# Kernel tuning notes

Hardware: AMD Instinct MI355X
Metric: run time of the kernel (lower is better)

The kernel has to match this reference:

```python
import jax, jax.numpy as jnp
import numpy as np

NUM_EMBEDDINGS = 1024
EMBEDDING_DIM = 256
COMMITMENT_COST = 0.25


def setup_inputs() -> dict:
    key = jax.random.key(0)
    k1, k2 = jax.random.split(key)
    x = jax.random.normal(k1, (16, 4096, EMBEDDING_DIM), dtype=jnp.float32)
    # torch init: uniform(-1/K, 1/K); keep same scale
    embedding_weight = jax.random.uniform(
        k2, (NUM_EMBEDDINGS, EMBEDDING_DIM), dtype=jnp.float32,
        minval=-1.0 / NUM_EMBEDDINGS, maxval=1.0 / NUM_EMBEDDINGS)
    return {"x": x, "embedding_weight": embedding_weight}


def reference(x, embedding_weight):
    original_shape = x.shape
    x_flat = x.reshape(-1, EMBEDDING_DIM)                     # [N, D]
    d2 = (jnp.sum(x_flat ** 2, axis=1, keepdims=True)
          + jnp.sum(embedding_weight ** 2, axis=1)
          - 2.0 * x_flat @ embedding_weight.T)                # [N, K]
    d2 = jnp.maximum(d2, 0.0)
    encoding_indices = jnp.argmin(d2, axis=1)                 # [N]
    quantized_flat = embedding_weight[encoding_indices]        # [N, D]
    quantized = quantized_flat.reshape(original_shape)

    q_sg = jax.lax.stop_gradient(quantized)
    codebook_loss = jnp.mean((q_sg - x) ** 2)
    commitment_loss = jnp.mean((x - q_sg) ** 2)
    vq_total_loss = codebook_loss + COMMITMENT_COST * commitment_loss

    # straight-through estimator
    quantized_st = x + jax.lax.stop_gradient(quantized - x)

    # perplexity via index counts (avoids materializing one-hot [N, K])
    n = x_flat.shape[0]
    counts = jnp.zeros((NUM_EMBEDDINGS,), jnp.float32).at[encoding_indices].add(1.0)
    avg_probs = counts / n
    perplexity = jnp.exp(-jnp.sum(avg_probs * jnp.log(avg_probs + 1e-10)))

    return quantized_st, vq_total_loss, perplexity, encoding_indices
```

## Files before the change

kernel.cpp:

```cpp
#include <hip/hip_runtime.h>
#include <math.h>

#define N_ROWS   65536
#define DIM      256
#define KCODES   1024
#define Q_SIZE   (N_ROWS * DIM)
#define OUT_LOSS Q_SIZE
#define OUT_PERP (Q_SIZE + 1)
#define OUT_IDX  (Q_SIZE + 2)

#define TAUP 200.0f

#define WS_LOSS   0
#define WS_RCNT   8
#define WS_E2     16
#define WS_E2P    4112
#define WS_COUNTS 8208
#define WS_IDX    12304
#define WS_RLIST  274448
#define WS_ET     536592
#define WS_P      1585168

typedef _Float16 half8 __attribute__((ext_vector_type(8)));
typedef _Float16 half4 __attribute__((ext_vector_type(4)));
typedef float    f32x4 __attribute__((ext_vector_type(4)));

#define ROWB 528
#define RPB  64

#define LDS_X  0
#define LDS_E2 33792

__global__ void k_prep(const float* __restrict__ E, float* __restrict__ e2,
                       float* __restrict__ e2p, float* __restrict__ Et,
                       _Float16* __restrict__ P,
                       int* __restrict__ counts, double* __restrict__ loss,
                       int* __restrict__ rcnt) {
    int b = blockIdx.x, t = threadIdx.x;
    __shared__ double red[256];
    float v = E[b * DIM + t];
    red[t] = (double)v * (double)v;

    {
        int o   = b * 256 + t;
        int j    = o & 7;
        int lane = (o >> 3) & 63;
        int nt   = (o >> 9) & 3;
        int kk   = (o >> 11) & 7;
        int cbq  = o >> 14;
        int q = cbq >> 2, cb = cbq & 3;
        int code = q * 256 + cb * 64 + nt * 16 + (lane & 15);
        int d    = (lane >> 4) * 8 + kk * 32 + j;
        P[o] = (_Float16)(E[code * DIM + d] * 1024.0f);
    }

    __syncthreads();
    for (int s = 128; s > 0; s >>= 1) {
        if (t < s) red[t] += red[t + s];
        __syncthreads();
    }
    if (t == 0) { e2[b] = (float)red[0]; e2p[b] = (float)(red[0] * 1048576.0); }

    int o = b * 256 + t;
    int d = o >> 10, k = o & 1023;
    Et[o] = E[k * DIM + d];

    if (b < 4) counts[b * 256 + t] = 0;
    if (b == 0 && t == 0) { *loss = 0.0; *rcnt = 0; }
}

__global__ void __launch_bounds__(256)
k_main(const float* __restrict__ X, const _Float16* __restrict__ P,
       const float* __restrict__ e2p,
       int* __restrict__ idx_ws, int* __restrict__ rlist,
       int* __restrict__ rcnt) {
    __shared__ __align__(16) char sAll[37888];
    const int tid  = threadIdx.x;
    const int wid  = tid >> 6;
    const int lane = tid & 63;
    const int c16  = lane & 15;
    const int kg   = lane >> 4;
    const int rb   = blockIdx.x * RPB;

    char* sA = sAll + LDS_X;

    {
        const f32x4* Xg = (const f32x4*)(X + (size_t)rb * DIM);
        #pragma unroll
        for (int it = 0; it < 16; ++it) {
            int f = it * 256 + tid;
            int row = f >> 6, d4 = f & 63;
            f32x4 v = __builtin_nontemporal_load(&Xg[(size_t)row * 64 + d4]);
            half4 hh = {(_Float16)v[0], (_Float16)v[1], (_Float16)v[2], (_Float16)v[3]};
            *(half4*)(sA + row * ROWB + d4 * 8) = hh;
        }
        ((f32x4*)(sAll + LDS_E2))[tid] = ((const f32x4*)e2p)[tid];
    }
    __syncthreads();

    const char* gB = (const char*)P + (size_t)wid * 131072 + (size_t)lane * 16;
#define GLOADC(dst, c)                                                        \
    asm volatile("global_load_dwordx4 %0, %1, off"                            \
                 : "=v"(dst)                                                  \
                 : "v"(gB + (size_t)((c) * 1024)))
#define VMW(n) { asm volatile("s_waitcnt vmcnt(" #n ")" ::: "memory");        \
                 __builtin_amdgcn_sched_barrier(0); }

    int Abase[4];
    #pragma unroll
    for (int mt = 0; mt < 4; ++mt) Abase[mt] = (mt * 16 + c16) * ROWB + kg * 16;

    float tb1[16], tb2[16];
    int   ti1[16];
    #pragma unroll
    for (int i = 0; i < 16; ++i) { tb1[i] = 3.4e38f; tb2[i] = 3.4e38f; ti1[i] = 0; }

    const int cw = wid * 256;
    const float* sE2 = (const float*)(sAll + LDS_E2);

    f32x4 acc[4][4];

    half8 b[3][4];
    #pragma unroll
    for (int nt = 0; nt < 4; ++nt) GLOADC(b[0][nt], 0 * 4 + nt);
    #pragma unroll
    for (int nt = 0; nt < 4; ++nt) GLOADC(b[1][nt], 1 * 4 + nt);
    __builtin_amdgcn_sched_barrier(0);

    #pragma unroll
    for (int s = 0; s < 32; ++s) {
        const int kk = s & 7;
        if (kk == 0) {
            #pragma unroll
            for (int mt = 0; mt < 4; ++mt)
                #pragma unroll
                for (int nt = 0; nt < 4; ++nt) acc[mt][nt] = 0.0f;
        }
        if (s <= 29) {
            #pragma unroll
            for (int nt = 0; nt < 4; ++nt) GLOADC(b[(s + 2) % 3][nt], (s + 2) * 4 + nt);
        }
        if (s <= 29)      VMW(8)
        else if (s == 30) VMW(4)
        else              VMW(0)

        half8 ah[4];
        #pragma unroll
        for (int mt = 0; mt < 4; ++mt)
            ah[mt] = *(const half8*)(sA + Abase[mt] + kk * 64);

        #pragma unroll
        for (int mt = 0; mt < 4; ++mt) {
            acc[mt][0] = __builtin_amdgcn_mfma_f32_16x16x32_f16(ah[mt], b[s % 3][0], acc[mt][0], 0, 0, 0);
            acc[mt][1] = __builtin_amdgcn_mfma_f32_16x16x32_f16(ah[mt], b[s % 3][1], acc[mt][1], 0, 0, 0);
            acc[mt][2] = __builtin_amdgcn_mfma_f32_16x16x32_f16(ah[mt], b[s % 3][2], acc[mt][2], 0, 0, 0);
            acc[mt][3] = __builtin_amdgcn_mfma_f32_16x16x32_f16(ah[mt], b[s % 3][3], acc[mt][3], 0, 0, 0);
        }

        if (kk == 7) {
            const int cb = s >> 3;
            const int cbase = cw + cb * 64;
            const int c0 = cbase + c16;
            float e2v[4];
            #pragma unroll
            for (int nt = 0; nt < 4; ++nt) e2v[nt] = sE2[c0 + nt * 16];
            #pragma unroll
            for (int mt = 0; mt < 4; ++mt)
                #pragma unroll
                for (int nt = 0; nt < 4; ++nt) {
                    int code = cbase + nt * 16 + c16;
                    #pragma unroll
                    for (int r = 0; r < 4; ++r) {
                        float sc = fmaf(-2048.0f, acc[mt][nt][r], e2v[nt]);
                        int ix = mt * 4 + r;
                        tb2[ix] = __builtin_amdgcn_fmed3f(tb1[ix], tb2[ix], sc);
                        bool lt = sc < tb1[ix];
                        tb1[ix] = lt ? sc : tb1[ix];
                        ti1[ix] = lt ? code : ti1[ix];
                    }
                }
        }
    }
#undef GLOADC
#undef VMW

    #pragma unroll
    for (int ix = 0; ix < 16; ++ix) {
        float v1 = tb1[ix], v2 = tb2[ix];
        int   j1 = ti1[ix];
        #pragma unroll
        for (int m = 1; m < 16; m <<= 1) {
            float ov1 = __shfl_xor(v1, m, 64);
            int   oj1 = __shfl_xor(j1, m, 64);
            float ov2 = __shfl_xor(v2, m, 64);
            bool take = (ov1 < v1) || (ov1 == v1 && oj1 < j1);
            float losr = take ? v1 : ov1;
            v1 = take ? ov1 : v1;
            j1 = take ? oj1 : j1;
            v2 = fminf(fminf(v2, ov2), losr);
        }
        tb1[ix] = v1; tb2[ix] = v2; ti1[ix] = j1;
    }

    __syncthreads();
    float* mB1 = (float*)sA;
    float* mB2 = (float*)(sA + 1024);
    int*   mI1 = (int*)(sA + 2048);
    #pragma unroll
    for (int ix = 0; ix < 16; ++ix) {
        if (c16 == ix) {
            int row = (ix >> 2) * 16 + kg * 4 + (ix & 3);
            mB1[row * 4 + wid] = tb1[ix];
            mB2[row * 4 + wid] = tb2[ix];
            mI1[row * 4 + wid] = ti1[ix];
        }
    }
    __syncthreads();
    if (tid < RPB) {
        float m1 = 3.4e38f, m2 = 3.4e38f;
        int mi = 0;
        #pragma unroll
        for (int w = 0; w < 4; ++w) {
            float v = mB1[tid * 4 + w];
            int  id = mI1[tid * 4 + w];
            float u = mB2[tid * 4 + w];
            bool take = (v < m1) || (v == m1 && id < mi);
            float losr = take ? m1 : v;
            m1 = take ? v : m1;
            mi = take ? id : mi;
            m2 = fminf(fminf(m2, u), losr);
        }
        int g = rb + tid;
        idx_ws[g] = mi;
        if (m2 - m1 < TAUP) {
            int slot = atomicAdd(rcnt, 1);
            rlist[slot] = g;
        }
    }
}

__launch_bounds__(256, 1)
__global__ void k_refine(const float* __restrict__ X, const float* __restrict__ Et,
                         const float* __restrict__ e2,
                         const int* __restrict__ rlist, const int* __restrict__ rcnt,
                         int* __restrict__ idx_ws) {
    __shared__ float xs[4][256];
    __shared__ float sbv[4][256];
    __shared__ int   sbi[4][256];
    __shared__ float x2s[4];
    __shared__ int   rows[4];
    const int cnt = *rcnt;
    const int t = threadIdx.x;
    for (int base = blockIdx.x * 4; base < cnt; base += gridDim.x * 4) {
        __syncthreads();
        if (t < 4) {
            int e = base + t;
            rows[t] = rlist[e < cnt ? e : (cnt - 1)];
        }
        __syncthreads();
        ((float4*)xs[t >> 6])[t & 63] =
            ((const float4*)(X + (size_t)rows[t >> 6] * DIM))[t & 63];
        __syncthreads();
        if (t < 4) {
            double s = 0.0;
            for (int d = 0; d < DIM; ++d) { double xv = (double)xs[t][d]; s += xv * xv; }
            x2s[t] = (float)s;
        }
        __syncthreads();

        double a0[4], a1[4], a2[4], a3[4];
        #pragma unroll
        for (int r = 0; r < 4; ++r) { a0[r] = 0.0; a1[r] = 0.0; a2[r] = 0.0; a3[r] = 0.0; }
        #pragma unroll 4
        for (int d = 0; d < DIM; ++d) {
            double e0 = (double)Et[d * KCODES + t];
            double e1 = (double)Et[d * KCODES + 256 + t];
            double e2d = (double)Et[d * KCODES + 512 + t];
            double e3 = (double)Et[d * KCODES + 768 + t];
            #pragma unroll
            for (int r = 0; r < 4; ++r) {
                double xv = (double)xs[r][d];
                a0[r] += xv * e0;
                a1[r] += xv * e1;
                a2[r] += xv * e2d;
                a3[r] += xv * e3;
            }
        }

        const float eA = e2[t], eB = e2[256 + t], eC = e2[512 + t], eD = e2[768 + t];
        #pragma unroll
        for (int r = 0; r < 4; ++r) {
            float best = 3.4e38f; int bk = 0;
            float x2 = x2s[r];
            { float d2 = fmaf(-2.f, (float)a0[r], x2 + eA); if (d2 < best) { best = d2; bk = t; } }
            { float d2 = fmaf(-2.f, (float)a1[r], x2 + eB); if (d2 < best) { best = d2; bk = 256 + t; } }
            { float d2 = fmaf(-2.f, (float)a2[r], x2 + eC); if (d2 < best) { best = d2; bk = 512 + t; } }
            { float d2 = fmaf(-2.f, (float)a3[r], x2 + eD); if (d2 < best) { best = d2; bk = 768 + t; } }
            sbv[r][t] = best; sbi[r][t] = bk;
        }
        __syncthreads();
        {
            const int w = t >> 6, lane = t & 63;
            float v = sbv[w][lane];     int id = sbi[w][lane];
            #pragma unroll
            for (int c = 1; c < 4; ++c) {
                float ov = sbv[w][lane + 64 * c]; int oi = sbi[w][lane + 64 * c];
                if (ov < v || (ov == v && oi < id)) { v = ov; id = oi; }
            }
            #pragma unroll
            for (int m = 1; m < 64; m <<= 1) {
                float ov = __shfl_xor(v, m, 64);
                int   oi = __shfl_xor(id, m, 64);
                if (ov < v || (ov == v && oi < id)) { v = ov; id = oi; }
            }
            if (lane == 0 && base + w < cnt) idx_ws[rows[w]] = id;
        }
    }
}

__launch_bounds__(256)
__global__ void k_out(const float* __restrict__ X, const float* __restrict__ E,
                      const int* __restrict__ idx_ws, float* __restrict__ out,
                      int* __restrict__ counts, double* __restrict__ loss) {
    const int tid = threadIdx.x;
    const int w = tid >> 6, lane = tid & 63;
    const int rbase = blockIdx.x * 64;
    double ls = 0.0;
    #pragma unroll 4
    for (int it = 0; it < 16; ++it) {
        const int row = rbase + it * 4 + w;
        const int k = idx_ws[row];
        float4 q = ((const float4*)(E + (size_t)k * DIM))[lane];
        float4 x = ((const float4*)(X + (size_t)row * DIM))[lane];
        ((float4*)(out + (size_t)row * DIM))[lane] = q;
        double d0 = (double)q.x - (double)x.x;
        double d1 = (double)q.y - (double)x.y;
        double d2 = (double)q.z - (double)x.z;
        double d3 = (double)q.w - (double)x.w;
        ls += d0 * d0 + d1 * d1 + d2 * d2 + d3 * d3;
        if (lane == 0) {
            atomicAdd(&counts[k], 1);
            out[OUT_IDX + row] = (float)k;
        }
    }
    __shared__ double red[256];
    red[tid] = ls;
    __syncthreads();
    for (int s = 128; s > 0; s >>= 1) {
        if (tid < s) red[tid] += red[tid + s];
        __syncthreads();
    }
    if (tid == 0) atomicAdd(loss, red[0]);
}

__global__ void k_fin(const int* __restrict__ counts, const double* __restrict__ loss,
                      float* __restrict__ out) {
    int t = threadIdx.x;
    __shared__ double red[256];
    double h = 0.0;
    #pragma unroll
    for (int i = 0; i < 4; ++i) {
        double p = (double)counts[t + i * 256] / (double)N_ROWS;
        h += p * log(p + 1e-10);
    }
    red[t] = h;
    __syncthreads();
    for (int s = 128; s > 0; s >>= 1) {
        if (t < s) red[t] += red[t + s];
        __syncthreads();
    }
    if (t == 0) {
        out[OUT_PERP] = (float)exp(-red[0]);
        out[OUT_LOSS] = (float)((*loss) / (double)Q_SIZE * 1.25);
    }
}

extern "C" void kernel_launch(void* const* d_in, const int* in_sizes, int n_in,
                              void* d_out, int out_size, void* d_ws, size_t ws_size,
                              hipStream_t stream) {
    (void)in_sizes; (void)n_in; (void)out_size; (void)ws_size;
    const float* X = (const float*)d_in[0];
    const float* E = (const float*)d_in[1];
    float* out = (float*)d_out;
    char* ws = (char*)d_ws;

    double*    loss   = (double*)(ws + WS_LOSS);
    int*       rcnt   = (int*)(ws + WS_RCNT);
    float*     e2     = (float*)(ws + WS_E2);
    float*     e2p    = (float*)(ws + WS_E2P);
    int*       counts = (int*)(ws + WS_COUNTS);
    int*       idx_ws = (int*)(ws + WS_IDX);
    int*       rlist  = (int*)(ws + WS_RLIST);
    float*     Et     = (float*)(ws + WS_ET);
    _Float16*  Pp     = (_Float16*)(ws + WS_P);

    k_prep<<<1024, 256, 0, stream>>>(E, e2, e2p, Et, Pp, counts, loss, rcnt);
    k_main<<<N_ROWS / RPB, 256, 0, stream>>>(X, Pp, e2p, idx_ws, rlist, rcnt);
    k_refine<<<1024, 256, 0, stream>>>(X, Et, e2, rlist, rcnt, idx_ws);
    k_out<<<1024, 256, 0, stream>>>(X, E, idx_ws, out, counts, loss);
    k_fin<<<1, 256, 0, stream>>>(counts, loss, out);
}
```

Measured before the change: 171.5 us.

## Split rows across waves and stage codebook tiles in LDS via global_load_lds

The main distance kernel changes from splitting the 1024 codes across waves (each wave covering all 64 rows) to splitting 128 rows across waves, where each wave covers all codes. The X fragments are kept in registers, and the codebook is streamed through a double-buffered LDS tile with direct global-to-LDS loads. This removes the cross-wave LDS merge of per-wave best and second-best results and halves the number of blocks, so each codebook load is shared by more rows. In exchange it needs a barrier every tile, keeps A fragments resident in registers (more VGPR pressure), and loads X into LDS in two phases.

```diff
diff --git a/kernel.cpp b/kernel.cpp
--- a/kernel.cpp
+++ b/kernel.cpp
@@ -26,9 +26,8 @@
 typedef float    f32x4 __attribute__((ext_vector_type(4)));
 
 #define ROWB 528
-#define RPB  64
-
-#define LDS_X  0
+#define RPB  128
+
 #define LDS_E2 33792
 
 __global__ void k_prep(const float* __restrict__ E, float* __restrict__ e2,
@@ -42,14 +41,13 @@
     red[t] = (double)v * (double)v;
 
     {
-        int o   = b * 256 + t;
+        int o    = b * 256 + t;
         int j    = o & 7;
         int lane = (o >> 3) & 63;
-        int nt   = (o >> 9) & 3;
-        int kk   = (o >> 11) & 7;
-        int cbq  = o >> 14;
-        int q = cbq >> 2, cb = cbq & 3;
-        int code = q * 256 + cb * 64 + nt * 16 + (lane & 15);
+        int c    = (o >> 9) & 15;
+        int T    = o >> 13;
+        int nt = c >> 3, kk = c & 7;
+        int code = T * 32 + nt * 16 + (lane & 15);
         int d    = (lane >> 4) * 8 + kk * 32 + j;
         P[o] = (_Float16)(E[code * DIM + d] * 1024.0f);
     }
@@ -82,7 +80,11 @@
     const int kg   = lane >> 4;
     const int rb   = blockIdx.x * RPB;
 
-    char* sA = sAll + LDS_X;
+    char* sX = sAll;
+    char* sB = sAll;
+    const float* sE2 = (const float*)(sAll + LDS_E2);
+
+    ((f32x4*)(sAll + LDS_E2))[tid] = ((const f32x4*)e2p)[tid];
 
     {
         const f32x4* Xg = (const f32x4*)(X + (size_t)rb * DIM);
@@ -92,100 +94,109 @@
             int row = f >> 6, d4 = f & 63;
             f32x4 v = __builtin_nontemporal_load(&Xg[(size_t)row * 64 + d4]);
             half4 hh = {(_Float16)v[0], (_Float16)v[1], (_Float16)v[2], (_Float16)v[3]};
-            *(half4*)(sA + row * ROWB + d4 * 8) = hh;
-        }
-        ((f32x4*)(sAll + LDS_E2))[tid] = ((const f32x4*)e2p)[tid];
-    }
-    __syncthreads();
-
-    const char* gB = (const char*)P + (size_t)wid * 131072 + (size_t)lane * 16;
-#define GLOADC(dst, c)                                                        \
-    asm volatile("global_load_dwordx4 %0, %1, off"                            \
-                 : "=v"(dst)                                                  \
-                 : "v"(gB + (size_t)((c) * 1024)))
-#define VMW(n) { asm volatile("s_waitcnt vmcnt(" #n ")" ::: "memory");        \
-                 __builtin_amdgcn_sched_barrier(0); }
-
-    int Abase[4];
+            *(half4*)(sX + row * ROWB + d4 * 8) = hh;
+        }
+    }
+    __syncthreads();
+    half8 ar[2][8];
+    if (wid < 2) {
+        #pragma unroll
+        for (int mt = 0; mt < 2; ++mt)
+            #pragma unroll
+            for (int kk = 0; kk < 8; ++kk)
+                ar[mt][kk] = *(const half8*)(sX + (wid * 32 + mt * 16 + c16) * ROWB
+                                             + kk * 64 + kg * 16);
+    }
+    __syncthreads();
+    {
+        const f32x4* Xg = (const f32x4*)(X + (size_t)(rb + 64) * DIM);
+        #pragma unroll
+        for (int it = 0; it < 16; ++it) {
+            int f = it * 256 + tid;
+            int row = f >> 6, d4 = f & 63;
+            f32x4 v = __builtin_nontemporal_load(&Xg[(size_t)row * 64 + d4]);
+            half4 hh = {(_Float16)v[0], (_Float16)v[1], (_Float16)v[2], (_Float16)v[3]};
+            *(half4*)(sX + row * ROWB + d4 * 8) = hh;
+        }
+    }
+    __syncthreads();
+    if (wid >= 2) {
+        #pragma unroll
+        for (int mt = 0; mt < 2; ++mt)
+            #pragma unroll
+            for (int kk = 0; kk < 8; ++kk)
+                ar[mt][kk] = *(const half8*)(sX + ((wid - 2) * 32 + mt * 16 + c16) * ROWB
+                                             + kk * 64 + kg * 16);
+    }
+    __syncthreads();
+
+#define STAGE(T)                                                                             \
+    {                                                                                        \
+        const char* src_ = (const char*)P + (size_t)(T) * 16384 + (size_t)(wid * 4) * 1024   \
+                           + (size_t)lane * 16;                                              \
+        char* dst_ = sB + ((T) & 1) * 16384 + (wid * 4) * 1024;                              \
+        __builtin_amdgcn_global_load_lds((const __attribute__((address_space(1))) unsigned int*)(src_),          \
+                                         (__attribute__((address_space(3))) unsigned int*)(dst_), 16, 0, 0);     \
+        __builtin_amdgcn_global_load_lds((const __attribute__((address_space(1))) unsigned int*)(src_ + 1024),   \
+                                         (__attribute__((address_space(3))) unsigned int*)(dst_ + 1024), 16, 0, 0);\
+        __builtin_amdgcn_global_load_lds((const __attribute__((address_space(1))) unsigned int*)(src_ + 2048),   \
+                                         (__attribute__((address_space(3))) unsigned int*)(dst_ + 2048), 16, 0, 0);\
+        __builtin_amdgcn_global_load_lds((const __attribute__((address_space(1))) unsigned int*)(src_ + 3072),   \
+                                         (__attribute__((address_space(3))) unsigned int*)(dst_ + 3072), 16, 0, 0);\
+    }
+
+    float tb1[8], tb2[8];
+    int   ti1[8];
     #pragma unroll
-    for (int mt = 0; mt < 4; ++mt) Abase[mt] = (mt * 16 + c16) * ROWB + kg * 16;
-
-    float tb1[16], tb2[16];
-    int   ti1[16];
+    for (int i = 0; i < 8; ++i) { tb1[i] = 3.4e38f; tb2[i] = 3.4e38f; ti1[i] = 0; }
+
+    f32x4 acc[2][2];
+
+    STAGE(0);
+    __syncthreads();
+
+    #pragma unroll 2
+    for (int T = 0; T < 32; ++T) {
+        if (T < 31) STAGE(T + 1);
+
+        #pragma unroll
+        for (int mt = 0; mt < 2; ++mt)
+            #pragma unroll
+            for (int nt = 0; nt < 2; ++nt) acc[mt][nt] = 0.0f;
+
+        const char* bbuf = sB + (T & 1) * 16384 + (size_t)lane * 16;
+        #pragma unroll
+        for (int kk = 0; kk < 8; ++kk) {
+            half8 b0 = *(const half8*)(bbuf + (0 * 8 + kk) * 1024);
+            half8 b1 = *(const half8*)(bbuf + (1 * 8 + kk) * 1024);
+            acc[0][0] = __builtin_amdgcn_mfma_f32_16x16x32_f16(ar[0][kk], b0, acc[0][0], 0, 0, 0);
+            acc[0][1] = __builtin_amdgcn_mfma_f32_16x16x32_f16(ar[0][kk], b1, acc[0][1], 0, 0, 0);
+            acc[1][0] = __builtin_amdgcn_mfma_f32_16x16x32_f16(ar[1][kk], b0, acc[1][0], 0, 0, 0);
+            acc[1][1] = __builtin_amdgcn_mfma_f32_16x16x32_f16(ar[1][kk], b1, acc[1][1], 0, 0, 0);
+        }
+
+        #pragma unroll
+        for (int nt = 0; nt < 2; ++nt) {
+            const int code = T * 32 + nt * 16 + c16;
+            const float e2v = sE2[code];
+            #pragma unroll
+            for (int mt = 0; mt < 2; ++mt)
+                #pragma unroll
+                for (int r = 0; r < 4; ++r) {
+                    float sc = fmaf(-2048.0f, acc[mt][nt][r], e2v);
+                    int ix = mt * 4 + r;
+                    tb2[ix] = __builtin_amdgcn_fmed3f(tb1[ix], tb2[ix], sc);
+                    bool lt = sc < tb1[ix];
+                    tb1[ix] = lt ? sc : tb1[ix];
+                    ti1[ix] = lt ? code : ti1[ix];
+                }
+        }
+        __syncthreads();
+    }
+#undef STAGE
+
     #pragma unroll
-    for (int i = 0; i < 16; ++i) { tb1[i] = 3.4e38f; tb2[i] = 3.4e38f; ti1[i] = 0; }
-
-    const int cw = wid * 256;
-    const float* sE2 = (const float*)(sAll + LDS_E2);
-
-    f32x4 acc[4][4];
-
-    half8 b[3][4];
-    #pragma unroll
-    for (int nt = 0; nt < 4; ++nt) GLOADC(b[0][nt], 0 * 4 + nt);
-    #pragma unroll
-    for (int nt = 0; nt < 4; ++nt) GLOADC(b[1][nt], 1 * 4 + nt);
-    __builtin_amdgcn_sched_barrier(0);
-
-    #pragma unroll
-    for (int s = 0; s < 32; ++s) {
-        const int kk = s & 7;
-        if (kk == 0) {
-            #pragma unroll
-            for (int mt = 0; mt < 4; ++mt)
-                #pragma unroll
-                for (int nt = 0; nt < 4; ++nt) acc[mt][nt] = 0.0f;
-        }
-        if (s <= 29) {
-            #pragma unroll
-            for (int nt = 0; nt < 4; ++nt) GLOADC(b[(s + 2) % 3][nt], (s + 2) * 4 + nt);
-        }
-        if (s <= 29)      VMW(8)
-        else if (s == 30) VMW(4)
-        else              VMW(0)
-
-        half8 ah[4];
-        #pragma unroll
-        for (int mt = 0; mt < 4; ++mt)
-            ah[mt] = *(const half8*)(sA + Abase[mt] + kk * 64);
-
-        #pragma unroll
-        for (int mt = 0; mt < 4; ++mt) {
-            acc[mt][0] = __builtin_amdgcn_mfma_f32_16x16x32_f16(ah[mt], b[s % 3][0], acc[mt][0], 0, 0, 0);
-            acc[mt][1] = __builtin_amdgcn_mfma_f32_16x16x32_f16(ah[mt], b[s % 3][1], acc[mt][1], 0, 0, 0);
-            acc[mt][2] = __builtin_amdgcn_mfma_f32_16x16x32_f16(ah[mt], b[s % 3][2], acc[mt][2], 0, 0, 0);
-            acc[mt][3] = __builtin_amdgcn_mfma_f32_16x16x32_f16(ah[mt], b[s % 3][3], acc[mt][3], 0, 0, 0);
-        }
-
-        if (kk == 7) {
-            const int cb = s >> 3;
-            const int cbase = cw + cb * 64;
-            const int c0 = cbase + c16;
-            float e2v[4];
-            #pragma unroll
-            for (int nt = 0; nt < 4; ++nt) e2v[nt] = sE2[c0 + nt * 16];
-            #pragma unroll
-            for (int mt = 0; mt < 4; ++mt)
-                #pragma unroll
-                for (int nt = 0; nt < 4; ++nt) {
-                    int code = cbase + nt * 16 + c16;
-                    #pragma unroll
-                    for (int r = 0; r < 4; ++r) {
-                        float sc = fmaf(-2048.0f, acc[mt][nt][r], e2v[nt]);
-                        int ix = mt * 4 + r;
-                        tb2[ix] = __builtin_amdgcn_fmed3f(tb1[ix], tb2[ix], sc);
-                        bool lt = sc < tb1[ix];
-                        tb1[ix] = lt ? sc : tb1[ix];
-                        ti1[ix] = lt ? code : ti1[ix];
-                    }
-                }
-        }
-    }
-#undef GLOADC
-#undef VMW
-
-    #pragma unroll
-    for (int ix = 0; ix < 16; ++ix) {
+    for (int ix = 0; ix < 8; ++ix) {
         float v1 = tb1[ix], v2 = tb2[ix];
         int   j1 = ti1[ix];
         #pragma unroll
@@ -201,40 +212,16 @@
         }
         tb1[ix] = v1; tb2[ix] = v2; ti1[ix] = j1;
     }
-
-    __syncthreads();
-    float* mB1 = (float*)sA;
-    float* mB2 = (float*)(sA + 1024);
-    int*   mI1 = (int*)(sA + 2048);
-    #pragma unroll
-    for (int ix = 0; ix < 16; ++ix) {
-        if (c16 == ix) {
-            int row = (ix >> 2) * 16 + kg * 4 + (ix & 3);
-            mB1[row * 4 + wid] = tb1[ix];
-            mB2[row * 4 + wid] = tb2[ix];
-            mI1[row * 4 + wid] = ti1[ix];
-        }
-    }
-    __syncthreads();
-    if (tid < RPB) {
-        float m1 = 3.4e38f, m2 = 3.4e38f;
-        int mi = 0;
-        #pragma unroll
-        for (int w = 0; w < 4; ++w) {
-            float v = mB1[tid * 4 + w];
-            int  id = mI1[tid * 4 + w];
-            float u = mB2[tid * 4 + w];
-            bool take = (v < m1) || (v == m1 && id < mi);
-            float losr = take ? m1 : v;
-            m1 = take ? v : m1;
-            mi = take ? id : mi;
-            m2 = fminf(fminf(m2, u), losr);
-        }
-        int g = rb + tid;
-        idx_ws[g] = mi;
-        if (m2 - m1 < TAUP) {
-            int slot = atomicAdd(rcnt, 1);
-            rlist[slot] = g;
+    if (c16 == 0) {
+        #pragma unroll
+        for (int ix = 0; ix < 8; ++ix) {
+            int row = wid * 32 + (ix >> 2) * 16 + kg * 4 + (ix & 3);
+            int g = rb + row;
+            idx_ws[g] = ti1[ix];
+            if (tb2[ix] - tb1[ix] < TAUP) {
+                int slot = atomicAdd(rcnt, 1);
+                rlist[slot] = g;
+            }
         }
     }
 }
```

Result: faster. 165.9 us (-3.3%).
